# Performance work log

Measured on AMD Instinct MI355X. Metric: run time of the kernel, lower is better.

## Reference

```python
import jax, jax.numpy as jnp
import numpy as np

# ---- config (matches init_kwargs) ----
GROUP_NUM = 2048
K_NEIGHBORS = 32
OUT_DIM = 192
SIGMA, BASELINE, SCALING, EPS = 0.26, 0.1, 10.0, 1e-6
ALPHA, BETA = 1000.0, 100.0
ADAPTIVE_RATIO = 0.5
IN_DIM = 3
ADAPTIVE_DIM = int(OUT_DIM * ADAPTIVE_RATIO)          # 96
FOURIER_DIM = OUT_DIM - ADAPTIVE_DIM                  # 96
FEAT_DIM_F = FOURIER_DIM // (IN_DIM * 2)              # 16
FEAT_DIM_A = int(np.ceil(ADAPTIVE_DIM / IN_DIM))      # 32
FEAT_NUM_A = FEAT_DIM_A * IN_DIM                      # 96
OUT_IDX = np.linspace(0, FEAT_NUM_A - 1, ADAPTIVE_DIM).astype(np.int64)


def setup_inputs() -> dict:
    key = jax.random.key(0)
    k1, k2, k3, k4 = jax.random.split(key, 4)
    xyz = jax.random.normal(k1, (4, 8192, 3), dtype=jnp.float32)
    x = jax.random.normal(k2, (4, 8192, 96), dtype=jnp.float32)
    bn_gamma = jax.random.uniform(k3, (192,), dtype=jnp.float32)
    bn_beta = jax.random.normal(k4, (192,), dtype=jnp.float32)
    return {"xyz": xyz, "x": x, "bn_gamma": bn_gamma, "bn_beta": bn_beta}


def _fps(xyz, m):
    """Farthest point sampling. xyz: [B,N,3] -> idx [B,m] (int32). Seed = index 0."""
    def single(pts):
        n = pts.shape[0]
        def step(carry, _):
            dists, last = carry
            d = jnp.sum((pts - pts[last]) ** 2, axis=-1)
            dists = jnp.minimum(dists, d)
            nxt = jnp.argmax(dists).astype(jnp.int32)
            return (dists, nxt), nxt
        init = (jnp.full((n,), 1e10, pts.dtype), jnp.array(0, jnp.int32))
        _, idxs = jax.lax.scan(step, init, None, length=m - 1)
        return jnp.concatenate([jnp.zeros((1,), jnp.int32), idxs])
    return jax.vmap(single)(xyz)


def _square_distance(src, dst):
    # src: [B,S,3], dst: [B,N,3] -> [B,S,N]
    d = -2.0 * jnp.einsum('bsc,bnc->bsn', src, dst)
    d += jnp.sum(src ** 2, -1)[:, :, None]
    d += jnp.sum(dst ** 2, -1)[:, None, :]
    return d


def _gather_knn(points, idx):
    # points: [B,N,C], idx: [B,G,K] -> [B,G,K,C]
    return jax.vmap(lambda p, i: p[i])(points, idx)


def _forward(xyz, x, bn_gamma, bn_beta):
    B, N, _ = xyz.shape
    G, K = GROUP_NUM, K_NEIGHBORS

    # ---- Grouper_seg ----
    fps_idx = _fps(xyz, G)                                   # [B,G]
    lc_xyz = jnp.take_along_axis(xyz, fps_idx[..., None], 1)  # [B,G,3]
    lc_x = jnp.take_along_axis(x, fps_idx[..., None], 1)      # [B,G,C]
    sqr = _square_distance(lc_xyz, xyz)                       # [B,G,N]
    knn_idx = jax.lax.top_k(-sqr, K)[1]                       # [B,G,K] smallest-k
    knn_xyz = _gather_knn(xyz, knn_idx)                       # [B,G,K,3]
    knn_x = _gather_knn(x, knn_idx)                           # [B,G,K,C]

    # ---- Aggregation_seg: local normalization ----
    mean_x = lc_x[:, :, None, :]
    std_x = jnp.std(knn_x - mean_x, ddof=1)
    mean_xyz = lc_xyz[:, :, None, :]
    std_xyz = jnp.std(knn_xyz - mean_xyz, ddof=1)
    knn_x = (knn_x - mean_x) / (std_x + 1e-5)
    knn_xyz_n = (knn_xyz - mean_xyz) / (std_xyz + 1e-5)       # [B,G,K,3]
    C = knn_x.shape[-1]
    knn_x = jnp.concatenate(
        [knn_x, jnp.broadcast_to(lc_x[:, :, None, :], (B, G, K, C))], axis=-1)  # [B,G,K,2C]
    knn_xyz_cf = jnp.transpose(knn_xyz_n, (0, 3, 1, 2))       # [B,3,G,K]
    knn_x_cf = jnp.transpose(knn_x, (0, 3, 1, 2))             # [B,OUT_DIM,G,K]

    # ---- PosE_Geo: fourier part ----
    feat_range = jnp.arange(FEAT_DIM_F, dtype=knn_xyz_cf.dtype)
    dim_embed = ALPHA ** (feat_range / FEAT_DIM_F)            # [F]
    div = BETA * knn_xyz_cf[..., None] / dim_embed            # [B,3,G,K,F]
    fourier = jnp.stack([jnp.sin(div), jnp.cos(div)], axis=-1)  # [B,3,G,K,F,2]
    fourier = fourier.reshape(B, IN_DIM, G, K, 2 * FEAT_DIM_F)
    fourier = jnp.transpose(fourier, (0, 1, 4, 2, 3)).reshape(B, FOURIER_DIM, G, K)

    # ---- AdaptiveEmbedding (parameterless, data-driven) ----
    x4 = knn_xyz_n                                            # [B,G,K,3]
    gstd = jnp.mean(jnp.std(x4.reshape(B, -1, IN_DIM), axis=1, ddof=1))
    sig = SIGMA * (1.0 + gstd) + EPS
    blend = jax.nn.sigmoid((gstd - BASELINE) * SCALING)
    feat_val = jnp.linspace(-1.0, 1.0, FEAT_DIM_A + 2)[1:-1]  # [Fa]
    z = (x4[..., None] - feat_val) / sig                      # [B,G,K,3,Fa]
    comb = blend * jnp.exp(-0.5 * z * z) + (1.0 - blend) * jnp.cos(z)
    ae = comb.reshape(B, G, K, FEAT_NUM_A)[..., OUT_IDX]      # [B,G,K,ADAPTIVE_DIM]
    ae_cf = jnp.transpose(ae, (0, 3, 1, 2))                   # [B,ADAPTIVE_DIM,G,K]

    pe = jnp.concatenate([fourier, ae_cf], axis=1)            # [B,OUT_DIM,G,K]
    knn_x_w = (knn_x_cf + pe) * pe

    # ---- Pooling_seg: max+mean pool, BatchNorm1d (train stats) + GELU ----
    lc = jnp.max(knn_x_w, -1) + jnp.mean(knn_x_w, -1)         # [B,OUT_DIM,G]
    mu = jnp.mean(lc, axis=(0, 2), keepdims=True)
    var = jnp.var(lc, axis=(0, 2), keepdims=True)
    y = (lc - mu) / jnp.sqrt(var + 1e-5)
    y = y * bn_gamma[None, :, None] + bn_beta[None, :, None]
    return jax.nn.gelu(y, approximate=False)


def reference(xyz, x, bn_gamma, bn_beta):
    return _forward(xyz, x, bn_gamma, bn_beta)
```

## Files before the change

kernel.cpp:

```cpp
#include <hip/hip_runtime.h>
#include <cstdint>
#include <math.h>

#define NPTS 8192
#define NB 4
#define NG 2048
#define NK 32
#define CIN 96
#define COUT 192

typedef unsigned long long ull;

__global__ __launch_bounds__(256) void setup_kernel(const float* __restrict__ xyz,
                                                    float* __restrict__ xs, float* __restrict__ ys,
                                                    float* __restrict__ zs, float* __restrict__ d2){
  int i = blockIdx.x*256 + threadIdx.x;
  if (i >= NB*NPTS) return;
  float x = xyz[3*i+0], y = xyz[3*i+1], z = xyz[3*i+2];
  xs[i]=x; ys[i]=y; zs[i]=z;
  d2[i] = __fadd_rn(__fadd_rn(__fmul_rn(x,x),__fmul_rn(y,y)),__fmul_rn(z,z));
}

template<int CTRL>
__device__ __forceinline__ void dppmax_pair(unsigned& hi, unsigned& lo){
  unsigned ohi = (unsigned)__builtin_amdgcn_update_dpp((int)hi, (int)hi, CTRL, 0xf, 0xf, false);
  unsigned olo = (unsigned)__builtin_amdgcn_update_dpp((int)lo, (int)lo, CTRL, 0xf, 0xf, false);
  bool gt = (ohi > hi) || (ohi == hi && olo > lo);
  hi = gt ? ohi : hi;
  lo = gt ? olo : lo;
}

__device__ __forceinline__ ull umax64(ull a, ull b){ return (a > b) ? a : b; }
__device__ __forceinline__ unsigned umax32(unsigned a, unsigned b){ return (a > b) ? a : b; }

__global__ __launch_bounds__(512,2) void fps_kernel(const float* __restrict__ xyz, int* __restrict__ fps_idx){
#pragma clang fp contract(off)
  extern __shared__ char smem[];
  float4* ctab = (float4*)smem;
  ull*    keys = (ull*)(smem + 131072);
  int*    hist = (int*)(smem + 131072 + 128);
  float*  bbs  = (float*)(smem + 131072 + 128 + 2048);
  const int b = blockIdx.x, t = threadIdx.x;
  const int w = t>>6, lane = t&63;
  const float* base = xyz + (size_t)b*NPTS*3;

  float ox[16], oy[16], oz[16];
#pragma unroll
  for (int j=0;j<16;++j){
    int p = t + 512*j;
    ox[j]=base[3*p+0]; oy[j]=base[3*p+1]; oz[j]=base[3*p+2];
  }
  float mnx=ox[0],mxx=ox[0],mny=oy[0],mxy=oy[0],mnz=oz[0],mxz=oz[0];
#pragma unroll
  for (int j=1;j<16;++j){
    mnx=fminf(mnx,ox[j]); mxx=fmaxf(mxx,ox[j]);
    mny=fminf(mny,oy[j]); mxy=fmaxf(mxy,oy[j]);
    mnz=fminf(mnz,oz[j]); mxz=fmaxf(mxz,oz[j]);
  }
#pragma unroll
  for (int off=32; off>0; off>>=1){
    mnx=fminf(mnx,__shfl_xor(mnx,off)); mxx=fmaxf(mxx,__shfl_xor(mxx,off));
    mny=fminf(mny,__shfl_xor(mny,off)); mxy=fmaxf(mxy,__shfl_xor(mxy,off));
    mnz=fminf(mnz,__shfl_xor(mnz,off)); mxz=fmaxf(mxz,__shfl_xor(mxz,off));
  }
  hist[t] = 0;
  if (lane==0){
    bbs[w*6+0]=mnx; bbs[w*6+1]=mxx; bbs[w*6+2]=mny;
    bbs[w*6+3]=mxy; bbs[w*6+4]=mnz; bbs[w*6+5]=mxz;
  }
  if (t==0) fps_idx[b*NG] = 0;
  __syncthreads();
  float gx0=1e30f,gx1=-1e30f,gy0=1e30f,gy1=-1e30f,gz0=1e30f,gz1=-1e30f;
  for (int q=0;q<8;++q){
    gx0=fminf(gx0,bbs[q*6+0]); gx1=fmaxf(gx1,bbs[q*6+1]);
    gy0=fminf(gy0,bbs[q*6+2]); gy1=fmaxf(gy1,bbs[q*6+3]);
    gz0=fminf(gz0,bbs[q*6+4]); gz1=fmaxf(gz1,bbs[q*6+5]);
  }
  const float sxv = 8.0f/fmaxf(gx1-gx0,1e-20f);
  const float syv = 8.0f/fmaxf(gy1-gy0,1e-20f);
  const float szv = 8.0f/fmaxf(gz1-gz0,1e-20f);
  int cell[16];
#pragma unroll
  for (int j=0;j<16;++j){
    int cx = min(7,(int)((ox[j]-gx0)*sxv));
    int cy = min(7,(int)((oy[j]-gy0)*syv));
    int cz = min(7,(int)((oz[j]-gz0)*szv));
    int m = (cx&1) | ((cy&1)<<1) | ((cz&1)<<2)
          | ((cx&2)<<2) | ((cy&2)<<3) | ((cz&2)<<4)
          | ((cx&4)<<4) | ((cy&4)<<5) | ((cz&4)<<6);
    cell[j]=m;
    atomicAdd(&hist[m],1);
  }
  __syncthreads();
  if (t < 64){
    int s0[8];
#pragma unroll
    for (int j=0;j<8;++j) s0[j]=hist[t*8+j];
    int tot=0;
#pragma unroll
    for (int j=0;j<8;++j){ int v=s0[j]; s0[j]=tot; tot+=v; }
    int inc=tot;
#pragma unroll
    for (int off=1; off<64; off<<=1){
      int o=__shfl_up(inc,off);
      if (t>=off) inc+=o;
    }
    int excl=inc-tot;
#pragma unroll
    for (int j=0;j<8;++j) hist[t*8+j]=excl+s0[j];
  }
  __syncthreads();
#pragma unroll
  for (int j=0;j<16;++j){
    int pos = atomicAdd(&hist[cell[j]],1);
    ctab[pos] = make_float4(ox[j],oy[j],oz[j], __int_as_float(t+512*j));
  }
  __syncthreads();
  float px[16],py[16],pz[16],D[16]; unsigned lowb[16];
  float bx0,bx1,by0,by1,bz0,bz1;
#pragma unroll
  for (int j=0;j<16;++j){
    int pos = (w<<10) + (j<<6) + lane;
    float4 c4 = ctab[pos];
    px[j]=c4.x; py[j]=c4.y; pz[j]=c4.z;
    unsigned orig = (unsigned)__float_as_int(c4.w);
    lowb[j] = ((8191u-orig)<<13) | (unsigned)pos;
    D[j] = 1e10f;
    if (j==0){ bx0=c4.x; bx1=c4.x; by0=c4.y; by1=c4.y; bz0=c4.z; bz1=c4.z; }
    else {
      bx0=fminf(bx0,c4.x); bx1=fmaxf(bx1,c4.x);
      by0=fminf(by0,c4.y); by1=fmaxf(by1,c4.y);
      bz0=fminf(bz0,c4.z); bz1=fmaxf(bz1,c4.z);
    }
  }
#pragma unroll
  for (int off=32; off>0; off>>=1){
    bx0=fminf(bx0,__shfl_xor(bx0,off)); bx1=fmaxf(bx1,__shfl_xor(bx1,off));
    by0=fminf(by0,__shfl_xor(by0,off)); by1=fmaxf(by1,__shfl_xor(by1,off));
    bz0=fminf(bz0,__shfl_xor(bz0,off)); bz1=fmaxf(bz1,__shfl_xor(bz1,off));
  }

  float lx=base[0], ly=base[1], lz=base[2];
  float Mw = 1e10f;
  unsigned mylow = 0;
  for (int it=0; it<NG-1; ++it){
    float qx=fminf(fmaxf(lx,bx0),bx1);
    float qy=fminf(fmaxf(ly,by0),by1);
    float qz=fminf(fmaxf(lz,bz0),bz1);
    float ddx=qx-lx, ddy=qy-ly, ddz=qz-lz;
    float LB = (ddx*ddx+ddy*ddy)+ddz*ddz;
    ull* kslot = &keys[(it&1)*8 + w];
    if (LB <= Mw*1.0001f){
#pragma unroll
      for (int j=0;j<16;++j){
        float dx=px[j]-lx, dy=py[j]-ly, dz=pz[j]-lz;
        float d=(dx*dx+dy*dy)+dz*dz;
        D[j]=fminf(D[j],d);
      }
      float m0=fmaxf(D[0],D[1]),   m1=fmaxf(D[2],D[3]);
      float m2=fmaxf(D[4],D[5]),   m3=fmaxf(D[6],D[7]);
      float m4=fmaxf(D[8],D[9]),   m5=fmaxf(D[10],D[11]);
      float m6=fmaxf(D[12],D[13]), m7=fmaxf(D[14],D[15]);
      float n0=fmaxf(m0,m1), n1=fmaxf(m2,m3), n2=fmaxf(m4,m5), n3=fmaxf(m6,m7);
      float bd=fmaxf(fmaxf(n0,n1),fmaxf(n2,n3));
      unsigned c[16];
#pragma unroll
      for (int j=0;j<16;++j) c[j] = (D[j]==bd) ? lowb[j] : 0u;
      unsigned u0=umax32(c[0],c[1]),   u1=umax32(c[2],c[3]);
      unsigned u2=umax32(c[4],c[5]),   u3=umax32(c[6],c[7]);
      unsigned u4=umax32(c[8],c[9]),   u5=umax32(c[10],c[11]);
      unsigned u6=umax32(c[12],c[13]), u7=umax32(c[14],c[15]);
      unsigned v0=umax32(u0,u1), v1=umax32(u2,u3), v2=umax32(u4,u5), v3=umax32(u6,u7);
      unsigned bl=umax32(umax32(v0,v1),umax32(v2,v3));
      unsigned hi = __float_as_uint(bd), lo = bl;
      dppmax_pair<0x111>(hi,lo); dppmax_pair<0x112>(hi,lo); dppmax_pair<0x114>(hi,lo);
      dppmax_pair<0x118>(hi,lo); dppmax_pair<0x142>(hi,lo); dppmax_pair<0x143>(hi,lo);
      unsigned hw  = (unsigned)__builtin_amdgcn_readlane((int)hi,63);
      unsigned lwv = (unsigned)__builtin_amdgcn_readlane((int)lo,63);
      if (lane==63) *kslot = (((ull)hw)<<32) | (ull)lwv;
      Mw = __uint_as_float(hw);
      mylow = lwv;
    } else {
      if (lane==63) *kslot = (((ull)__float_as_uint(Mw))<<32) | (ull)mylow;
    }
    __syncthreads();
    const ulonglong2* kk2 = (const ulonglong2*)(keys + (it&1)*8);
    ulonglong2 p0 = kk2[0], p1 = kk2[1], p2 = kk2[2], p3 = kk2[3];
    ull a0 = umax64(p0.x, p0.y), a1 = umax64(p1.x, p1.y);
    ull a2 = umax64(p2.x, p2.y), a3 = umax64(p3.x, p3.y);
    ull k  = umax64(umax64(a0,a1), umax64(a2,a3));
    unsigned lw = (unsigned)k;
    float4 c4 = ctab[lw & 0x1FFFu];
    lx=c4.x; ly=c4.y; lz=c4.z;
    if (t==0) fps_idx[b*NG + it + 1] = (int)(8191u - ((lw>>13)&0x1FFFu));
  }
}

__device__ __forceinline__ bool lexlt(float ad, int ai, float bd, int bi){
  return (ad < bd) || ((ad == bd) && (ai < bi));
}
__device__ __forceinline__ void sort_desc(float& d, int& i, int lane){
#pragma unroll
  for (int k=2;k<=64;k<<=1){
#pragma unroll
    for (int j=k>>1;j>0;j>>=1){
      float od = __shfl_xor(d, j);
      int   oi = __shfl_xor(i, j);
      bool dirUp = (lane & k) != 0;
      bool lower = (lane & j) == 0;
      bool less  = lexlt(d,i,od,oi);
      bool keep  = (less == (lower == dirUp));
      if (!keep){ d=od; i=oi; }
    }
  }
}
__device__ __forceinline__ void merge_asc(float& d, int& i, int lane){
#pragma unroll
  for (int j=32;j>0;j>>=1){
    float od = __shfl_xor(d, j);
    int   oi = __shfl_xor(i, j);
    bool lower = (lane & j) == 0;
    bool less  = lexlt(d,i,od,oi);
    bool keep  = (less == lower);
    if (!keep){ d=od; i=oi; }
  }
}

__global__ __launch_bounds__(256) void knn_kernel(const float* __restrict__ xs, const float* __restrict__ ys,
                                                  const float* __restrict__ zs, const float* __restrict__ d2,
                                                  const int* __restrict__ fps_idx, int* __restrict__ knn_out){
  __shared__ float tx[256], ty[256], tz[256], td[256];
  const int tid = threadIdx.x;
  const int wid = tid>>6, lane = tid&63;
  const int pid = blockIdx.x*4 + wid;
  const int b = pid >> 11;
  const float* bx = xs + b*NPTS;
  const float* by = ys + b*NPTS;
  const float* bz = zs + b*NPTS;
  const float* bD = d2 + b*NPTS;
  const int fi = fps_idx[pid];
  const float ax = bx[fi], ay = by[fi], az = bz[fi];
  const float src2 = __fadd_rn(__fadd_rn(__fmul_rn(ax,ax),__fmul_rn(ay,ay)),__fmul_rn(az,az));
  float Ad = INFINITY; int Ai = 0x7fffffff;
  float tau_d = INFINITY; int tau_i = 0x7fffffff;
  for (int s=0; s<NPTS/256; ++s){
    __syncthreads();
    int gidx = s*256 + tid;
    tx[tid]=bx[gidx]; ty[tid]=by[gidx]; tz[tid]=bz[gidx]; td[tid]=bD[gidx];
    __syncthreads();
    float m0,m1,m2,m3; int i0,i1,i2,i3;
#define LOADJ(mj, ij, J) { int li = (J)*64 + lane; \
    float dot = __fadd_rn(__fadd_rn(__fmul_rn(ax,tx[li]),__fmul_rn(ay,ty[li])),__fmul_rn(az,tz[li])); \
    mj = __fadd_rn(__fadd_rn(__fmul_rn(-2.0f,dot), src2), td[li]); ij = s*256 + li; }
    LOADJ(m0,i0,0) LOADJ(m1,i1,1) LOADJ(m2,i2,2) LOADJ(m3,i3,3)
#undef LOADJ
    while (true){
      bool any = lexlt(m0,i0,tau_d,tau_i) || lexlt(m1,i1,tau_d,tau_i) ||
                 lexlt(m2,i2,tau_d,tau_i) || lexlt(m3,i3,tau_d,tau_i);
      if (__ballot(any) == 0ull) break;
      float cd = m0; int ci = i0; int sel = 0;
      if (lexlt(m1,i1,cd,ci)){ cd=m1; ci=i1; sel=1; }
      if (lexlt(m2,i2,cd,ci)){ cd=m2; ci=i2; sel=2; }
      if (lexlt(m3,i3,cd,ci)){ cd=m3; ci=i3; sel=3; }
      if      (sel==0) m0=INFINITY;
      else if (sel==1) m1=INFINITY;
      else if (sel==2) m2=INFINITY;
      else             m3=INFINITY;
      sort_desc(cd, ci, lane);
      if (lexlt(cd,ci,Ad,Ai)){ Ad=cd; Ai=ci; }
      merge_asc(Ad, Ai, lane);
      tau_d = __shfl(Ad, 31);
      tau_i = __shfl(Ai, 31);
    }
  }
  if (lane < NK) knn_out[pid*NK + lane] = Ai;
}

__global__ __launch_bounds__(256) void stats_kernel(const float* __restrict__ x, const float* __restrict__ xyz,
                                                    const int* __restrict__ fps_idx, const int* __restrict__ knn,
                                                    double* __restrict__ partials){
  const int tid=threadIdx.x, wid=tid>>6, lane=tid&63;
  const int pid = blockIdx.x*4 + wid;
  const int b = pid>>11;
  const int fi = fps_idx[pid];
  const float* xb = x + (size_t)b*NPTS*CIN;
  const float* zb = xyz + (size_t)b*NPTS*3;
  const float lc0 = xb[fi*CIN + lane];
  float lc1 = 0.f; if (lane<32) lc1 = xb[fi*CIN + 64 + lane];
  float czv = 0.f; if (lane<3)  czv = zb[fi*3 + lane];
  double s1=0.0, s2=0.0, a1=0.0, a2=0.0;
  for (int k=0;k<NK;++k){
    int idx = knn[pid*NK + k];
    float d0 = __fsub_rn(xb[idx*CIN + lane], lc0);
    s1 += (double)d0; s2 += (double)d0*(double)d0;
    if (lane<32){
      float d1 = __fsub_rn(xb[idx*CIN + 64 + lane], lc1);
      s1 += (double)d1; s2 += (double)d1*(double)d1;
    }
    if (lane<3){
      float w = __fsub_rn(zb[idx*3 + lane], czv);
      a1 += (double)w; a2 += (double)w*(double)w;
    }
  }
#pragma unroll
  for (int off=32; off>0; off>>=1){ s1 += __shfl_xor(s1,off); s2 += __shfl_xor(s2,off); }
  __shared__ double shx[4][2];
  __shared__ double shz[4][3][2];
  if (lane==0){ shx[wid][0]=s1; shx[wid][1]=s2; }
  if (lane<3){ shz[wid][lane][0]=a1; shz[wid][lane][1]=a2; }
  __syncthreads();
  if (tid==0){
    double u0=0,u1=0;
    for (int w=0;w<4;++w){ u0+=shx[w][0]; u1+=shx[w][1]; }
    double* outp = partials + (size_t)blockIdx.x*8;
    outp[0]=u0; outp[1]=u1;
    for (int axq=0; axq<3; ++axq){
      double v0=0,v1=0;
      for (int w=0;w<4;++w){ v0+=shz[w][axq][0]; v1+=shz[w][axq][1]; }
      outp[2+2*axq]=v0; outp[3+2*axq]=v1;
    }
  }
}

__global__ void finalize_kernel(const double* __restrict__ partials, float* __restrict__ scal){
  const int lane = threadIdx.x;
  double s1=0,s2=0;
  double z0a=0,z0b=0,z1a=0,z1b=0,z2a=0,z2b=0;
  for (int i=0;i<32;++i){
    const double* p = partials + (size_t)(lane*32+i)*8;
    s1+=p[0]; s2+=p[1];
    z0a+=p[2]; z0b+=p[3]; z1a+=p[4]; z1b+=p[5]; z2a+=p[6]; z2b+=p[7];
  }
#pragma unroll
  for (int off=32; off>0; off>>=1){ s1+=__shfl_xor(s1,off); s2+=__shfl_xor(s2,off); }
#pragma unroll
  for (int off=8; off>0; off>>=1){
    z0a+=__shfl_xor(z0a,off); z0b+=__shfl_xor(z0b,off);
    z1a+=__shfl_xor(z1a,off); z1b+=__shfl_xor(z1b,off);
    z2a+=__shfl_xor(z2a,off); z2b+=__shfl_xor(z2b,off);
  }
  __shared__ double zb[4][3][2];
  if ((lane&15)==0){
    int b = lane>>4;
    zb[b][0][0]=z0a; zb[b][0][1]=z0b;
    zb[b][1][0]=z1a; zb[b][1][1]=z1b;
    zb[b][2][0]=z2a; zb[b][2][1]=z2b;
  }
  __syncthreads();
  if (lane==0){
    double nx = (double)NB*NG*NK*CIN;
    double varx = (s2 - s1*s1/nx)/(nx-1.0);
    float stdx = (float)sqrt(varx);
    double t1=0,t2=0;
    for (int b=0;b<4;++b) for (int a=0;a<3;++a){ t1+=zb[b][a][0]; t2+=zb[b][a][1]; }
    double nz = (double)NB*NG*NK*3;
    double varz = (t2 - t1*t1/nz)/(nz-1.0);
    float stdz = (float)sqrt(varz);
    float sdiv = stdz + 1e-5f;
    double n2 = (double)NG*NK;
    double acc=0.0;
    for (int b=0;b<4;++b) for (int a=0;a<3;++a){
      double v = (zb[b][a][1] - zb[b][a][0]*zb[b][a][0]/n2)/(n2-1.0);
      acc += sqrt(v);
    }
    float gstd = (float)(acc/12.0) / sdiv;
    float sig = 0.26f*(1.0f+gstd) + 1e-6f;
    float blend = 1.0f/(1.0f + expf(-(gstd-0.1f)*10.0f));
    scal[0] = 1.0f/(stdx + 1e-5f);
    scal[1] = 1.0f/sdiv;
    scal[2] = 1.0f/sig;
    scal[3] = blend;
  }
}

__global__ __launch_bounds__(256) void main_kernel(const float* __restrict__ x, const float* __restrict__ xyz,
                                                   const int* __restrict__ fps_idx, const int* __restrict__ knn,
                                                   const float* __restrict__ scal, float* __restrict__ lc_out){
  const int tid=threadIdx.x, wid=tid>>6, lane=tid&63;
  const int pid = blockIdx.x*4 + wid;
  const int b = pid>>11, g = pid&2047;
  const float inv_x = scal[0], inv_z = scal[1], inv_sig = scal[2], blend = scal[3];
  const float omb = 1.0f - blend;
  const int fi = fps_idx[pid];
  const float* xb = x + (size_t)b*NPTS*CIN;
  const float* zb = xyz + (size_t)b*NPTS*3;
  const float cx = zb[fi*3+0], cy = zb[fi*3+1], cz = zb[fi*3+2];
  const float lcx0 = xb[fi*CIN + lane];
  const float lcx1 = (lane<32) ? xb[fi*CIN + 64 + lane] : xb[fi*CIN + lane - 32];
  const float lcx2 = xb[fi*CIN + 32 + lane];
  const int dim0 = lane>>5;
  const int rr0 = lane&31;
  const bool cos0 = rr0 & 1;
  const float bs0 = 100.0f / powf(1000.0f, (float)(rr0>>1) * (1.0f/16.0f));
  const bool cos1 = lane & 1;
  const float bs1 = 100.0f / powf(1000.0f, (float)((lane&31)>>1) * (1.0f/16.0f));
  const float fv1 = (float)(-1.0 + 2.0*(double)(lane-32+1)/33.0);
  const int dim2 = (32+lane)>>5;
  const int j2 = (32+lane)&31;
  const float fv2 = (float)(-1.0 + 2.0*(double)(j2+1)/33.0);

  float mx0=-INFINITY, mx1=-INFINITY, mx2=-INFINITY;
  float sm0=0.f, sm1=0.f, sm2=0.f;
  for (int k=0;k<NK;++k){
    const int idx = knn[pid*NK + k];
    const float p0 = zb[idx*3+0], p1 = zb[idx*3+1], p2v = zb[idx*3+2];
    const float xn0 = (p0-cx)*inv_z, xn1 = (p1-cy)*inv_z, xn2 = (p2v-cz)*inv_z;
    const float xk0 = xb[idx*CIN + lane];
    float xk1 = 0.f; if (lane<32) xk1 = xb[idx*CIN + 64 + lane];
    {
      float v = dim0 ? xn1 : xn0;
      float a = v * bs0;
      float pe = cos0 ? __cosf(a) : __sinf(a);
      float f = (xk0 - lcx0) * inv_x;
      float w = (f + pe) * pe;
      mx0 = fmaxf(mx0, w); sm0 += w;
    }
    {
      float pe, f;
      if (lane < 32){
        float a = xn2 * bs1;
        pe = cos1 ? __cosf(a) : __sinf(a);
        f = (xk1 - lcx1) * inv_x;
      } else {
        float zq = (xn0 - fv1) * inv_sig;
        pe = blend * __expf(-0.5f*zq*zq) + omb * __cosf(zq);
        f = lcx1;
      }
      float w = (f + pe) * pe;
      mx1 = fmaxf(mx1, w); sm1 += w;
    }
    {
      float v = (dim2==1) ? xn1 : xn2;
      float zq = (v - fv2) * inv_sig;
      float pe = blend * __expf(-0.5f*zq*zq) + omb * __cosf(zq);
      float w = (lcx2 + pe) * pe;
      mx2 = fmaxf(mx2, w); sm2 += w;
    }
  }
  const size_t obase = ((size_t)b*COUT)*NG + g;
  lc_out[obase + (size_t)lane*NG]       = mx0 + sm0*(1.0f/32.0f);
  lc_out[obase + (size_t)(64+lane)*NG]  = mx1 + sm1*(1.0f/32.0f);
  lc_out[obase + (size_t)(128+lane)*NG] = mx2 + sm2*(1.0f/32.0f);
}

__global__ __launch_bounds__(256) void bn_stats_kernel(const float* __restrict__ lc, float* __restrict__ bn){
  const int c = blockIdx.x, t = threadIdx.x, lane=t&63, wid=t>>6;
  double s1=0.0, s2=0.0;
  for (int i=t; i<NB*NG; i+=256){
    int b=i>>11, g=i&2047;
    float v = lc[((size_t)(b*COUT)+c)*NG + g];
    s1 += (double)v; s2 += (double)v*(double)v;
  }
#pragma unroll
  for (int off=32; off>0; off>>=1){ s1+=__shfl_xor(s1,off); s2+=__shfl_xor(s2,off); }
  __shared__ double sh1[4], sh2[4];
  if (lane==0){ sh1[wid]=s1; sh2[wid]=s2; }
  __syncthreads();
  if (t==0){
    double a=sh1[0]+sh1[1]+sh1[2]+sh1[3], q=sh2[0]+sh2[1]+sh2[2]+sh2[3];
    double n=(double)(NB*NG);
    double mu=a/n, var=q/n - mu*mu;
    bn[c]=(float)mu;
    bn[COUT+c]=(float)(1.0/sqrt(var + 1e-5));
  }
}

__global__ __launch_bounds__(256) void final_kernel(const float* __restrict__ bn, const float* __restrict__ gamma,
                                                    const float* __restrict__ beta, float* __restrict__ out){
  int i = blockIdx.x*256 + threadIdx.x;
  int c = (i >> 11) % COUT;
  float v = out[i];
  float y = (v - bn[c]) * bn[COUT + c];
  y = y*gamma[c] + beta[c];
  out[i] = y * 0.5f * (1.0f + erff(y * 0.70710678118654752f));
}

extern "C" void kernel_launch(void* const* d_in, const int* in_sizes, int n_in,
                              void* d_out, int out_size, void* d_ws, size_t ws_size,
                              hipStream_t stream){
  const float* xyz   = (const float*)d_in[0];
  const float* x     = (const float*)d_in[1];
  const float* gamma = (const float*)d_in[2];
  const float* beta  = (const float*)d_in[3];
  float* out = (float*)d_out;
  char* ws = (char*)d_ws;
  int*    fps  = (int*)   (ws + 0);
  int*    knn  = (int*)   (ws + 32768);
  float*  xs   = (float*) (ws + 1081344);
  float*  ys   = (float*) (ws + 1212416);
  float*  zs   = (float*) (ws + 1343488);
  float*  d2   = (float*) (ws + 1474560);
  double* parts= (double*)(ws + 1605632);
  float*  scal = (float*) (ws + 1736704);
  float*  bn   = (float*) (ws + 1736768);

  const int fps_lds = 131072 + 128 + 2048 + 192;
  (void)hipFuncSetAttribute(reinterpret_cast<const void*>(fps_kernel),
                            hipFuncAttributeMaxDynamicSharedMemorySize, fps_lds);

  setup_kernel   <<<dim3((NB*NPTS+255)/256), dim3(256), 0, stream>>>(xyz, xs, ys, zs, d2);
  fps_kernel     <<<dim3(NB),                dim3(512), fps_lds, stream>>>(xyz, fps);
  knn_kernel     <<<dim3(NB*NG/4),           dim3(256), 0, stream>>>(xs, ys, zs, d2, fps, knn);
  stats_kernel   <<<dim3(NB*NG/4),           dim3(256), 0, stream>>>(x, xyz, fps, knn, parts);
  finalize_kernel<<<dim3(1),                 dim3(64),  0, stream>>>(parts, scal);
  main_kernel    <<<dim3(NB*NG/4),           dim3(256), 0, stream>>>(x, xyz, fps, knn, scal, out);
  bn_stats_kernel<<<dim3(COUT),              dim3(256), 0, stream>>>(out, bn);
  final_kernel   <<<dim3((NB*COUT*NG)/256),  dim3(256), 0, stream>>>(bn, gamma, beta, out);
}
```

Before: 2.476 ms.

## Fuse FPS, KNN and stats into one ticketed kernel that overlaps FPS

Replaces the separate FPS, KNN and stats kernels with one kernel whose blocks take roles from an atomic ticket counter. The first four blocks run farthest point sampling and publish progress flags every 16 samples. The remaining blocks spin until their 8 centroids are ready, then run KNN and the per-group feature statistics, reading neighbour indices directly from registers. The aim is to hide KNN and stats behind the long serial FPS loop and drop two launches plus the knn index reload. The cost is that waiting blocks hold CUs with large LDS reservations, the design depends on ticket ordering for forward progress, and the partials ordering changes, so finalize is adjusted to match.

```diff
diff --git a/kernel.cpp b/kernel.cpp
--- a/kernel.cpp
+++ b/kernel.cpp
@@ -13,8 +13,10 @@
 
 __global__ __launch_bounds__(256) void setup_kernel(const float* __restrict__ xyz,
                                                     float* __restrict__ xs, float* __restrict__ ys,
-                                                    float* __restrict__ zs, float* __restrict__ d2){
+                                                    float* __restrict__ zs, float* __restrict__ d2,
+                                                    int* __restrict__ ctrs){
   int i = blockIdx.x*256 + threadIdx.x;
+  if (i < 8){ ctrs[i] = 0; }
   if (i >= NB*NPTS) return;
   float x = xyz[3*i+0], y = xyz[3*i+1], z = xyz[3*i+2];
   xs[i]=x; ys[i]=y; zs[i]=z;
@@ -32,169 +34,6 @@
 
 __device__ __forceinline__ ull umax64(ull a, ull b){ return (a > b) ? a : b; }
 __device__ __forceinline__ unsigned umax32(unsigned a, unsigned b){ return (a > b) ? a : b; }
-
-__global__ __launch_bounds__(512,2) void fps_kernel(const float* __restrict__ xyz, int* __restrict__ fps_idx){
-#pragma clang fp contract(off)
-  extern __shared__ char smem[];
-  float4* ctab = (float4*)smem;
-  ull*    keys = (ull*)(smem + 131072);
-  int*    hist = (int*)(smem + 131072 + 128);
-  float*  bbs  = (float*)(smem + 131072 + 128 + 2048);
-  const int b = blockIdx.x, t = threadIdx.x;
-  const int w = t>>6, lane = t&63;
-  const float* base = xyz + (size_t)b*NPTS*3;
-
-  float ox[16], oy[16], oz[16];
-#pragma unroll
-  for (int j=0;j<16;++j){
-    int p = t + 512*j;
-    ox[j]=base[3*p+0]; oy[j]=base[3*p+1]; oz[j]=base[3*p+2];
-  }
-  float mnx=ox[0],mxx=ox[0],mny=oy[0],mxy=oy[0],mnz=oz[0],mxz=oz[0];
-#pragma unroll
-  for (int j=1;j<16;++j){
-    mnx=fminf(mnx,ox[j]); mxx=fmaxf(mxx,ox[j]);
-    mny=fminf(mny,oy[j]); mxy=fmaxf(mxy,oy[j]);
-    mnz=fminf(mnz,oz[j]); mxz=fmaxf(mxz,oz[j]);
-  }
-#pragma unroll
-  for (int off=32; off>0; off>>=1){
-    mnx=fminf(mnx,__shfl_xor(mnx,off)); mxx=fmaxf(mxx,__shfl_xor(mxx,off));
-    mny=fminf(mny,__shfl_xor(mny,off)); mxy=fmaxf(mxy,__shfl_xor(mxy,off));
-    mnz=fminf(mnz,__shfl_xor(mnz,off)); mxz=fmaxf(mxz,__shfl_xor(mxz,off));
-  }
-  hist[t] = 0;
-  if (lane==0){
-    bbs[w*6+0]=mnx; bbs[w*6+1]=mxx; bbs[w*6+2]=mny;
-    bbs[w*6+3]=mxy; bbs[w*6+4]=mnz; bbs[w*6+5]=mxz;
-  }
-  if (t==0) fps_idx[b*NG] = 0;
-  __syncthreads();
-  float gx0=1e30f,gx1=-1e30f,gy0=1e30f,gy1=-1e30f,gz0=1e30f,gz1=-1e30f;
-  for (int q=0;q<8;++q){
-    gx0=fminf(gx0,bbs[q*6+0]); gx1=fmaxf(gx1,bbs[q*6+1]);
-    gy0=fminf(gy0,bbs[q*6+2]); gy1=fmaxf(gy1,bbs[q*6+3]);
-    gz0=fminf(gz0,bbs[q*6+4]); gz1=fmaxf(gz1,bbs[q*6+5]);
-  }
-  const float sxv = 8.0f/fmaxf(gx1-gx0,1e-20f);
-  const float syv = 8.0f/fmaxf(gy1-gy0,1e-20f);
-  const float szv = 8.0f/fmaxf(gz1-gz0,1e-20f);
-  int cell[16];
-#pragma unroll
-  for (int j=0;j<16;++j){
-    int cx = min(7,(int)((ox[j]-gx0)*sxv));
-    int cy = min(7,(int)((oy[j]-gy0)*syv));
-    int cz = min(7,(int)((oz[j]-gz0)*szv));
-    int m = (cx&1) | ((cy&1)<<1) | ((cz&1)<<2)
-          | ((cx&2)<<2) | ((cy&2)<<3) | ((cz&2)<<4)
-          | ((cx&4)<<4) | ((cy&4)<<5) | ((cz&4)<<6);
-    cell[j]=m;
-    atomicAdd(&hist[m],1);
-  }
-  __syncthreads();
-  if (t < 64){
-    int s0[8];
-#pragma unroll
-    for (int j=0;j<8;++j) s0[j]=hist[t*8+j];
-    int tot=0;
-#pragma unroll
-    for (int j=0;j<8;++j){ int v=s0[j]; s0[j]=tot; tot+=v; }
-    int inc=tot;
-#pragma unroll
-    for (int off=1; off<64; off<<=1){
-      int o=__shfl_up(inc,off);
-      if (t>=off) inc+=o;
-    }
-    int excl=inc-tot;
-#pragma unroll
-    for (int j=0;j<8;++j) hist[t*8+j]=excl+s0[j];
-  }
-  __syncthreads();
-#pragma unroll
-  for (int j=0;j<16;++j){
-    int pos = atomicAdd(&hist[cell[j]],1);
-    ctab[pos] = make_float4(ox[j],oy[j],oz[j], __int_as_float(t+512*j));
-  }
-  __syncthreads();
-  float px[16],py[16],pz[16],D[16]; unsigned lowb[16];
-  float bx0,bx1,by0,by1,bz0,bz1;
-#pragma unroll
-  for (int j=0;j<16;++j){
-    int pos = (w<<10) + (j<<6) + lane;
-    float4 c4 = ctab[pos];
-    px[j]=c4.x; py[j]=c4.y; pz[j]=c4.z;
-    unsigned orig = (unsigned)__float_as_int(c4.w);
-    lowb[j] = ((8191u-orig)<<13) | (unsigned)pos;
-    D[j] = 1e10f;
-    if (j==0){ bx0=c4.x; bx1=c4.x; by0=c4.y; by1=c4.y; bz0=c4.z; bz1=c4.z; }
-    else {
-      bx0=fminf(bx0,c4.x); bx1=fmaxf(bx1,c4.x);
-      by0=fminf(by0,c4.y); by1=fmaxf(by1,c4.y);
-      bz0=fminf(bz0,c4.z); bz1=fmaxf(bz1,c4.z);
-    }
-  }
-#pragma unroll
-  for (int off=32; off>0; off>>=1){
-    bx0=fminf(bx0,__shfl_xor(bx0,off)); bx1=fmaxf(bx1,__shfl_xor(bx1,off));
-    by0=fminf(by0,__shfl_xor(by0,off)); by1=fmaxf(by1,__shfl_xor(by1,off));
-    bz0=fminf(bz0,__shfl_xor(bz0,off)); bz1=fmaxf(bz1,__shfl_xor(bz1,off));
-  }
-
-  float lx=base[0], ly=base[1], lz=base[2];
-  float Mw = 1e10f;
-  unsigned mylow = 0;
-  for (int it=0; it<NG-1; ++it){
-    float qx=fminf(fmaxf(lx,bx0),bx1);
-    float qy=fminf(fmaxf(ly,by0),by1);
-    float qz=fminf(fmaxf(lz,bz0),bz1);
-    float ddx=qx-lx, ddy=qy-ly, ddz=qz-lz;
-    float LB = (ddx*ddx+ddy*ddy)+ddz*ddz;
-    ull* kslot = &keys[(it&1)*8 + w];
-    if (LB <= Mw*1.0001f){
-#pragma unroll
-      for (int j=0;j<16;++j){
-        float dx=px[j]-lx, dy=py[j]-ly, dz=pz[j]-lz;
-        float d=(dx*dx+dy*dy)+dz*dz;
-        D[j]=fminf(D[j],d);
-      }
-      float m0=fmaxf(D[0],D[1]),   m1=fmaxf(D[2],D[3]);
-      float m2=fmaxf(D[4],D[5]),   m3=fmaxf(D[6],D[7]);
-      float m4=fmaxf(D[8],D[9]),   m5=fmaxf(D[10],D[11]);
-      float m6=fmaxf(D[12],D[13]), m7=fmaxf(D[14],D[15]);
-      float n0=fmaxf(m0,m1), n1=fmaxf(m2,m3), n2=fmaxf(m4,m5), n3=fmaxf(m6,m7);
-      float bd=fmaxf(fmaxf(n0,n1),fmaxf(n2,n3));
-      unsigned c[16];
-#pragma unroll
-      for (int j=0;j<16;++j) c[j] = (D[j]==bd) ? lowb[j] : 0u;
-      unsigned u0=umax32(c[0],c[1]),   u1=umax32(c[2],c[3]);
-      unsigned u2=umax32(c[4],c[5]),   u3=umax32(c[6],c[7]);
-      unsigned u4=umax32(c[8],c[9]),   u5=umax32(c[10],c[11]);
-      unsigned u6=umax32(c[12],c[13]), u7=umax32(c[14],c[15]);
-      unsigned v0=umax32(u0,u1), v1=umax32(u2,u3), v2=umax32(u4,u5), v3=umax32(u6,u7);
-      unsigned bl=umax32(umax32(v0,v1),umax32(v2,v3));
-      unsigned hi = __float_as_uint(bd), lo = bl;
-      dppmax_pair<0x111>(hi,lo); dppmax_pair<0x112>(hi,lo); dppmax_pair<0x114>(hi,lo);
-      dppmax_pair<0x118>(hi,lo); dppmax_pair<0x142>(hi,lo); dppmax_pair<0x143>(hi,lo);
-      unsigned hw  = (unsigned)__builtin_amdgcn_readlane((int)hi,63);
-      unsigned lwv = (unsigned)__builtin_amdgcn_readlane((int)lo,63);
-      if (lane==63) *kslot = (((ull)hw)<<32) | (ull)lwv;
-      Mw = __uint_as_float(hw);
-      mylow = lwv;
-    } else {
-      if (lane==63) *kslot = (((ull)__float_as_uint(Mw))<<32) | (ull)mylow;
-    }
-    __syncthreads();
-    const ulonglong2* kk2 = (const ulonglong2*)(keys + (it&1)*8);
-    ulonglong2 p0 = kk2[0], p1 = kk2[1], p2 = kk2[2], p3 = kk2[3];
-    ull a0 = umax64(p0.x, p0.y), a1 = umax64(p1.x, p1.y);
-    ull a2 = umax64(p2.x, p2.y), a3 = umax64(p3.x, p3.y);
-    ull k  = umax64(umax64(a0,a1), umax64(a2,a3));
-    unsigned lw = (unsigned)k;
-    float4 c4 = ctab[lw & 0x1FFFu];
-    lx=c4.x; ly=c4.y; lz=c4.z;
-    if (t==0) fps_idx[b*NG + it + 1] = (int)(8191u - ((lw>>13)&0x1FFFu));
-  }
-}
 
 __device__ __forceinline__ bool lexlt(float ad, int ai, float bd, int bi){
   return (ad < bd) || ((ad == bd) && (ai < bi));
@@ -226,98 +65,292 @@
   }
 }
 
-__global__ __launch_bounds__(256) void knn_kernel(const float* __restrict__ xs, const float* __restrict__ ys,
-                                                  const float* __restrict__ zs, const float* __restrict__ d2,
-                                                  const int* __restrict__ fps_idx, int* __restrict__ knn_out){
-  __shared__ float tx[256], ty[256], tz[256], td[256];
-  const int tid = threadIdx.x;
-  const int wid = tid>>6, lane = tid&63;
-  const int pid = blockIdx.x*4 + wid;
-  const int b = pid >> 11;
-  const float* bx = xs + b*NPTS;
-  const float* by = ys + b*NPTS;
-  const float* bz = zs + b*NPTS;
-  const float* bD = d2 + b*NPTS;
-  const int fi = fps_idx[pid];
-  const float ax = bx[fi], ay = by[fi], az = bz[fi];
-  const float src2 = __fadd_rn(__fadd_rn(__fmul_rn(ax,ax),__fmul_rn(ay,ay)),__fmul_rn(az,az));
-  float Ad = INFINITY; int Ai = 0x7fffffff;
-  float tau_d = INFINITY; int tau_i = 0x7fffffff;
-  for (int s=0; s<NPTS/256; ++s){
+__global__ __launch_bounds__(512,2) void mega_kernel(const float* __restrict__ xyz,
+                                                     const float* __restrict__ x,
+                                                     const float* __restrict__ xs,
+                                                     const float* __restrict__ ys,
+                                                     const float* __restrict__ zs,
+                                                     const float* __restrict__ d2,
+                                                     int* __restrict__ fps_idx,
+                                                     int* __restrict__ knn_out,
+                                                     double* __restrict__ partials,
+                                                     int* __restrict__ ctrs){
+  extern __shared__ char smem[];
+  __shared__ int role_s;
+  const int t = threadIdx.x;
+  const int w = t>>6, lane = t&63;
+  if (t==0) role_s = atomicAdd(&ctrs[0], 1);
+  __syncthreads();
+  const int ticket = role_s;
+
+  if (ticket < NB){
+#pragma clang fp contract(off)
+    float4* ctab = (float4*)smem;
+    ull*    keys = (ull*)(smem + 131072);
+    int*    hist = (int*)(smem + 131072 + 128);
+    float*  bbs  = (float*)(smem + 131072 + 128 + 2048);
+    const int b = ticket;
+    const float* base = xyz + (size_t)b*NPTS*3;
+
+    float ox[16], oy[16], oz[16];
+#pragma unroll
+    for (int j=0;j<16;++j){
+      int p = t + 512*j;
+      ox[j]=base[3*p+0]; oy[j]=base[3*p+1]; oz[j]=base[3*p+2];
+    }
+    float mnx=ox[0],mxx=ox[0],mny=oy[0],mxy=oy[0],mnz=oz[0],mxz=oz[0];
+#pragma unroll
+    for (int j=1;j<16;++j){
+      mnx=fminf(mnx,ox[j]); mxx=fmaxf(mxx,ox[j]);
+      mny=fminf(mny,oy[j]); mxy=fmaxf(mxy,oy[j]);
+      mnz=fminf(mnz,oz[j]); mxz=fmaxf(mxz,oz[j]);
+    }
+#pragma unroll
+    for (int off=32; off>0; off>>=1){
+      mnx=fminf(mnx,__shfl_xor(mnx,off)); mxx=fmaxf(mxx,__shfl_xor(mxx,off));
+      mny=fminf(mny,__shfl_xor(mny,off)); mxy=fmaxf(mxy,__shfl_xor(mxy,off));
+      mnz=fminf(mnz,__shfl_xor(mnz,off)); mxz=fmaxf(mxz,__shfl_xor(mxz,off));
+    }
+    hist[t] = 0;
+    if (lane==0){
+      bbs[w*6+0]=mnx; bbs[w*6+1]=mxx; bbs[w*6+2]=mny;
+      bbs[w*6+3]=mxy; bbs[w*6+4]=mnz; bbs[w*6+5]=mxz;
+    }
+    if (t==0) fps_idx[b*NG] = 0;
     __syncthreads();
-    int gidx = s*256 + tid;
-    tx[tid]=bx[gidx]; ty[tid]=by[gidx]; tz[tid]=bz[gidx]; td[tid]=bD[gidx];
+    float gx0=1e30f,gx1=-1e30f,gy0=1e30f,gy1=-1e30f,gz0=1e30f,gz1=-1e30f;
+    for (int q=0;q<8;++q){
+      gx0=fminf(gx0,bbs[q*6+0]); gx1=fmaxf(gx1,bbs[q*6+1]);
+      gy0=fminf(gy0,bbs[q*6+2]); gy1=fmaxf(gy1,bbs[q*6+3]);
+      gz0=fminf(gz0,bbs[q*6+4]); gz1=fmaxf(gz1,bbs[q*6+5]);
+    }
+    const float sxv = 8.0f/fmaxf(gx1-gx0,1e-20f);
+    const float syv = 8.0f/fmaxf(gy1-gy0,1e-20f);
+    const float szv = 8.0f/fmaxf(gz1-gz0,1e-20f);
+    int cell[16];
+#pragma unroll
+    for (int j=0;j<16;++j){
+      int cx = min(7,(int)((ox[j]-gx0)*sxv));
+      int cy = min(7,(int)((oy[j]-gy0)*syv));
+      int cz = min(7,(int)((oz[j]-gz0)*szv));
+      int m = (cx&1) | ((cy&1)<<1) | ((cz&1)<<2)
+            | ((cx&2)<<2) | ((cy&2)<<3) | ((cz&2)<<4)
+            | ((cx&4)<<4) | ((cy&4)<<5) | ((cz&4)<<6);
+      cell[j]=m;
+      atomicAdd(&hist[m],1);
+    }
     __syncthreads();
-    float m0,m1,m2,m3; int i0,i1,i2,i3;
+    if (t < 64){
+      int s0[8];
+#pragma unroll
+      for (int j=0;j<8;++j) s0[j]=hist[t*8+j];
+      int tot=0;
+#pragma unroll
+      for (int j=0;j<8;++j){ int v=s0[j]; s0[j]=tot; tot+=v; }
+      int inc=tot;
+#pragma unroll
+      for (int off=1; off<64; off<<=1){
+        int o=__shfl_up(inc,off);
+        if (t>=off) inc+=o;
+      }
+      int excl=inc-tot;
+#pragma unroll
+      for (int j=0;j<8;++j) hist[t*8+j]=excl+s0[j];
+    }
+    __syncthreads();
+#pragma unroll
+    for (int j=0;j<16;++j){
+      int pos = atomicAdd(&hist[cell[j]],1);
+      ctab[pos] = make_float4(ox[j],oy[j],oz[j], __int_as_float(t+512*j));
+    }
+    __syncthreads();
+    float px[16],py[16],pz[16],D[16]; unsigned lowb[16];
+    float bx0,bx1,by0,by1,bz0,bz1;
+#pragma unroll
+    for (int j=0;j<16;++j){
+      int pos = (w<<10) + (j<<6) + lane;
+      float4 c4 = ctab[pos];
+      px[j]=c4.x; py[j]=c4.y; pz[j]=c4.z;
+      unsigned orig = (unsigned)__float_as_int(c4.w);
+      lowb[j] = ((8191u-orig)<<13) | (unsigned)pos;
+      D[j] = 1e10f;
+      if (j==0){ bx0=c4.x; bx1=c4.x; by0=c4.y; by1=c4.y; bz0=c4.z; bz1=c4.z; }
+      else {
+        bx0=fminf(bx0,c4.x); bx1=fmaxf(bx1,c4.x);
+        by0=fminf(by0,c4.y); by1=fmaxf(by1,c4.y);
+        bz0=fminf(bz0,c4.z); bz1=fmaxf(bz1,c4.z);
+      }
+    }
+#pragma unroll
+    for (int off=32; off>0; off>>=1){
+      bx0=fminf(bx0,__shfl_xor(bx0,off)); bx1=fmaxf(bx1,__shfl_xor(bx1,off));
+      by0=fminf(by0,__shfl_xor(by0,off)); by1=fmaxf(by1,__shfl_xor(by1,off));
+      bz0=fminf(bz0,__shfl_xor(bz0,off)); bz1=fmaxf(bz1,__shfl_xor(bz1,off));
+    }
+
+    float lx=base[0], ly=base[1], lz=base[2];
+    float Mw = 1e10f;
+    unsigned mylow = 0;
+    for (int it=0; it<NG-1; ++it){
+      float qx=fminf(fmaxf(lx,bx0),bx1);
+      float qy=fminf(fmaxf(ly,by0),by1);
+      float qz=fminf(fmaxf(lz,bz0),bz1);
+      float ddx=qx-lx, ddy=qy-ly, ddz=qz-lz;
+      float LB = (ddx*ddx+ddy*ddy)+ddz*ddz;
+      ull* kslot = &keys[(it&1)*8 + w];
+      if (LB <= Mw*1.0001f){
+#pragma unroll
+        for (int j=0;j<16;++j){
+          float dx=px[j]-lx, dy=py[j]-ly, dz=pz[j]-lz;
+          float d=(dx*dx+dy*dy)+dz*dz;
+          D[j]=fminf(D[j],d);
+        }
+        float m0=fmaxf(D[0],D[1]),   m1=fmaxf(D[2],D[3]);
+        float m2=fmaxf(D[4],D[5]),   m3=fmaxf(D[6],D[7]);
+        float m4=fmaxf(D[8],D[9]),   m5=fmaxf(D[10],D[11]);
+        float m6=fmaxf(D[12],D[13]), m7=fmaxf(D[14],D[15]);
+        float n0=fmaxf(m0,m1), n1=fmaxf(m2,m3), n2=fmaxf(m4,m5), n3=fmaxf(m6,m7);
+        float bd=fmaxf(fmaxf(n0,n1),fmaxf(n2,n3));
+        unsigned c[16];
+#pragma unroll
+        for (int j=0;j<16;++j) c[j] = (D[j]==bd) ? lowb[j] : 0u;
+        unsigned u0=umax32(c[0],c[1]),   u1=umax32(c[2],c[3]);
+        unsigned u2=umax32(c[4],c[5]),   u3=umax32(c[6],c[7]);
+        unsigned u4=umax32(c[8],c[9]),   u5=umax32(c[10],c[11]);
+        unsigned u6=umax32(c[12],c[13]), u7=umax32(c[14],c[15]);
+        unsigned v0=umax32(u0,u1), v1=umax32(u2,u3), v2=umax32(u4,u5), v3=umax32(u6,u7);
+        unsigned bl=umax32(umax32(v0,v1),umax32(v2,v3));
+        unsigned hi = __float_as_uint(bd), lo = bl;
+        dppmax_pair<0x111>(hi,lo); dppmax_pair<0x112>(hi,lo); dppmax_pair<0x114>(hi,lo);
+        dppmax_pair<0x118>(hi,lo); dppmax_pair<0x142>(hi,lo); dppmax_pair<0x143>(hi,lo);
+        unsigned hw  = (unsigned)__builtin_amdgcn_readlane((int)hi,63);
+        unsigned lwv = (unsigned)__builtin_amdgcn_readlane((int)lo,63);
+        if (lane==63) *kslot = (((ull)hw)<<32) | (ull)lwv;
+        Mw = __uint_as_float(hw);
+        mylow = lwv;
+      } else {
+        if (lane==63) *kslot = (((ull)__float_as_uint(Mw))<<32) | (ull)mylow;
+      }
+      __syncthreads();
+      const ulonglong2* kk2 = (const ulonglong2*)(keys + (it&1)*8);
+      ulonglong2 p0 = kk2[0], p1 = kk2[1], p2 = kk2[2], p3 = kk2[3];
+      ull a0 = umax64(p0.x, p0.y), a1 = umax64(p1.x, p1.y);
+      ull a2 = umax64(p2.x, p2.y), a3 = umax64(p3.x, p3.y);
+      ull k  = umax64(umax64(a0,a1), umax64(a2,a3));
+      unsigned lw = (unsigned)k;
+      float4 c4 = ctab[lw & 0x1FFFu];
+      lx=c4.x; ly=c4.y; lz=c4.z;
+      if (t==0){
+        fps_idx[b*NG + it + 1] = (int)(8191u - ((lw>>13)&0x1FFFu));
+        if (((it+2)&15)==0)
+          __hip_atomic_store(&ctrs[1+b], it+2, __ATOMIC_RELEASE, __HIP_MEMORY_SCOPE_AGENT);
+      }
+    }
+  } else {
+    const int cc = ticket - NB;
+    const int b  = cc & 3;
+    const int chunk = cc >> 2;
+    const int g0 = chunk*8;
+    if (t==0){
+      while (__hip_atomic_load(&ctrs[1+b], __ATOMIC_ACQUIRE, __HIP_MEMORY_SCOPE_AGENT) < g0+8)
+        __builtin_amdgcn_s_sleep(8);
+    }
+    __syncthreads();
+    const int g   = g0 + w;
+    const int pid = b*NG + g;
+    const int fi  = fps_idx[pid];
+
+    float* tx = (float*)smem;
+    float* ty = tx + 512;
+    float* tz = ty + 512;
+    float* td = tz + 512;
+    const float* bx = xs + b*NPTS;
+    const float* by = ys + b*NPTS;
+    const float* bz = zs + b*NPTS;
+    const float* bD = d2 + b*NPTS;
+    const float ax = bx[fi], ay = by[fi], az = bz[fi];
+    const float src2 = __fadd_rn(__fadd_rn(__fmul_rn(ax,ax),__fmul_rn(ay,ay)),__fmul_rn(az,az));
+    float Ad = INFINITY; int Ai = 0x7fffffff;
+    float tau_d = INFINITY; int tau_i = 0x7fffffff;
+    for (int s=0; s<NPTS/512; ++s){
+      __syncthreads();
+      int gidx = s*512 + t;
+      tx[t]=bx[gidx]; ty[t]=by[gidx]; tz[t]=bz[gidx]; td[t]=bD[gidx];
+      __syncthreads();
+      float m0,m1,m2,m3,m4,m5,m6,m7; int i0,i1,i2,i3,i4,i5,i6,i7;
 #define LOADJ(mj, ij, J) { int li = (J)*64 + lane; \
-    float dot = __fadd_rn(__fadd_rn(__fmul_rn(ax,tx[li]),__fmul_rn(ay,ty[li])),__fmul_rn(az,tz[li])); \
-    mj = __fadd_rn(__fadd_rn(__fmul_rn(-2.0f,dot), src2), td[li]); ij = s*256 + li; }
-    LOADJ(m0,i0,0) LOADJ(m1,i1,1) LOADJ(m2,i2,2) LOADJ(m3,i3,3)
+      float dot = __fadd_rn(__fadd_rn(__fmul_rn(ax,tx[li]),__fmul_rn(ay,ty[li])),__fmul_rn(az,tz[li])); \
+      mj = __fadd_rn(__fadd_rn(__fmul_rn(-2.0f,dot), src2), td[li]); ij = s*512 + li; }
+      LOADJ(m0,i0,0) LOADJ(m1,i1,1) LOADJ(m2,i2,2) LOADJ(m3,i3,3)
+      LOADJ(m4,i4,4) LOADJ(m5,i5,5) LOADJ(m6,i6,6) LOADJ(m7,i7,7)
 #undef LOADJ
-    while (true){
-      bool any = lexlt(m0,i0,tau_d,tau_i) || lexlt(m1,i1,tau_d,tau_i) ||
-                 lexlt(m2,i2,tau_d,tau_i) || lexlt(m3,i3,tau_d,tau_i);
-      if (__ballot(any) == 0ull) break;
-      float cd = m0; int ci = i0; int sel = 0;
-      if (lexlt(m1,i1,cd,ci)){ cd=m1; ci=i1; sel=1; }
-      if (lexlt(m2,i2,cd,ci)){ cd=m2; ci=i2; sel=2; }
-      if (lexlt(m3,i3,cd,ci)){ cd=m3; ci=i3; sel=3; }
-      if      (sel==0) m0=INFINITY;
-      else if (sel==1) m1=INFINITY;
-      else if (sel==2) m2=INFINITY;
-      else             m3=INFINITY;
-      sort_desc(cd, ci, lane);
-      if (lexlt(cd,ci,Ad,Ai)){ Ad=cd; Ai=ci; }
-      merge_asc(Ad, Ai, lane);
-      tau_d = __shfl(Ad, 31);
-      tau_i = __shfl(Ai, 31);
-    }
-  }
-  if (lane < NK) knn_out[pid*NK + lane] = Ai;
-}
-
-__global__ __launch_bounds__(256) void stats_kernel(const float* __restrict__ x, const float* __restrict__ xyz,
-                                                    const int* __restrict__ fps_idx, const int* __restrict__ knn,
-                                                    double* __restrict__ partials){
-  const int tid=threadIdx.x, wid=tid>>6, lane=tid&63;
-  const int pid = blockIdx.x*4 + wid;
-  const int b = pid>>11;
-  const int fi = fps_idx[pid];
-  const float* xb = x + (size_t)b*NPTS*CIN;
-  const float* zb = xyz + (size_t)b*NPTS*3;
-  const float lc0 = xb[fi*CIN + lane];
-  float lc1 = 0.f; if (lane<32) lc1 = xb[fi*CIN + 64 + lane];
-  float czv = 0.f; if (lane<3)  czv = zb[fi*3 + lane];
-  double s1=0.0, s2=0.0, a1=0.0, a2=0.0;
-  for (int k=0;k<NK;++k){
-    int idx = knn[pid*NK + k];
-    float d0 = __fsub_rn(xb[idx*CIN + lane], lc0);
-    s1 += (double)d0; s2 += (double)d0*(double)d0;
-    if (lane<32){
-      float d1 = __fsub_rn(xb[idx*CIN + 64 + lane], lc1);
-      s1 += (double)d1; s2 += (double)d1*(double)d1;
-    }
-    if (lane<3){
-      float w = __fsub_rn(zb[idx*3 + lane], czv);
-      a1 += (double)w; a2 += (double)w*(double)w;
-    }
-  }
-#pragma unroll
-  for (int off=32; off>0; off>>=1){ s1 += __shfl_xor(s1,off); s2 += __shfl_xor(s2,off); }
-  __shared__ double shx[4][2];
-  __shared__ double shz[4][3][2];
-  if (lane==0){ shx[wid][0]=s1; shx[wid][1]=s2; }
-  if (lane<3){ shz[wid][lane][0]=a1; shz[wid][lane][1]=a2; }
-  __syncthreads();
-  if (tid==0){
-    double u0=0,u1=0;
-    for (int w=0;w<4;++w){ u0+=shx[w][0]; u1+=shx[w][1]; }
-    double* outp = partials + (size_t)blockIdx.x*8;
-    outp[0]=u0; outp[1]=u1;
-    for (int axq=0; axq<3; ++axq){
-      double v0=0,v1=0;
-      for (int w=0;w<4;++w){ v0+=shz[w][axq][0]; v1+=shz[w][axq][1]; }
-      outp[2+2*axq]=v0; outp[3+2*axq]=v1;
+      while (true){
+        bool any = lexlt(m0,i0,tau_d,tau_i) || lexlt(m1,i1,tau_d,tau_i) ||
+                   lexlt(m2,i2,tau_d,tau_i) || lexlt(m3,i3,tau_d,tau_i) ||
+                   lexlt(m4,i4,tau_d,tau_i) || lexlt(m5,i5,tau_d,tau_i) ||
+                   lexlt(m6,i6,tau_d,tau_i) || lexlt(m7,i7,tau_d,tau_i);
+        if (__ballot(any) == 0ull) break;
+        float cd = m0; int ci = i0; int sel = 0;
+        if (lexlt(m1,i1,cd,ci)){ cd=m1; ci=i1; sel=1; }
+        if (lexlt(m2,i2,cd,ci)){ cd=m2; ci=i2; sel=2; }
+        if (lexlt(m3,i3,cd,ci)){ cd=m3; ci=i3; sel=3; }
+        if (lexlt(m4,i4,cd,ci)){ cd=m4; ci=i4; sel=4; }
+        if (lexlt(m5,i5,cd,ci)){ cd=m5; ci=i5; sel=5; }
+        if (lexlt(m6,i6,cd,ci)){ cd=m6; ci=i6; sel=6; }
+        if (lexlt(m7,i7,cd,ci)){ cd=m7; ci=i7; sel=7; }
+        if      (sel==0) m0=INFINITY;
+        else if (sel==1) m1=INFINITY;
+        else if (sel==2) m2=INFINITY;
+        else if (sel==3) m3=INFINITY;
+        else if (sel==4) m4=INFINITY;
+        else if (sel==5) m5=INFINITY;
+        else if (sel==6) m6=INFINITY;
+        else             m7=INFINITY;
+        sort_desc(cd, ci, lane);
+        if (lexlt(cd,ci,Ad,Ai)){ Ad=cd; Ai=ci; }
+        merge_asc(Ad, Ai, lane);
+        tau_d = __shfl(Ad, 31);
+        tau_i = __shfl(Ai, 31);
+      }
+    }
+    if (lane < NK) knn_out[pid*NK + lane] = Ai;
+
+    const float* xb  = x   + (size_t)b*NPTS*CIN;
+    const float* zbp = xyz + (size_t)b*NPTS*3;
+    const float lc0 = xb[fi*CIN + lane];
+    float lc1 = 0.f; if (lane<32) lc1 = xb[fi*CIN + 64 + lane];
+    float czv = 0.f; if (lane<3)  czv = zbp[fi*3 + lane];
+    double s1=0.0, s2=0.0, a1=0.0, a2=0.0;
+    for (int kk=0;kk<NK;++kk){
+      int idx = __shfl(Ai, kk);
+      float d0 = __fsub_rn(xb[idx*CIN + lane], lc0);
+      s1 += (double)d0; s2 += (double)d0*(double)d0;
+      if (lane<32){
+        float d1 = __fsub_rn(xb[idx*CIN + 64 + lane], lc1);
+        s1 += (double)d1; s2 += (double)d1*(double)d1;
+      }
+      if (lane<3){
+        float wv = __fsub_rn(zbp[idx*3 + lane], czv);
+        a1 += (double)wv; a2 += (double)wv*(double)wv;
+      }
+    }
+#pragma unroll
+    for (int off=32; off>0; off>>=1){ s1 += __shfl_xor(s1,off); s2 += __shfl_xor(s2,off); }
+    __shared__ double shx[8][2];
+    __shared__ double shz[8][3][2];
+    if (lane==0){ shx[w][0]=s1; shx[w][1]=s2; }
+    if (lane<3){ shz[w][lane][0]=a1; shz[w][lane][1]=a2; }
+    __syncthreads();
+    if (t==0){
+      double u0=0,u1=0;
+      for (int q=0;q<8;++q){ u0+=shx[q][0]; u1+=shx[q][1]; }
+      double* outp = partials + (size_t)cc*8;
+      outp[0]=u0; outp[1]=u1;
+      for (int axq=0; axq<3; ++axq){
+        double v0=0,v1=0;
+        for (int q=0;q<8;++q){ v0+=shz[q][axq][0]; v1+=shz[q][axq][1]; }
+        outp[2+2*axq]=v0; outp[3+2*axq]=v1;
+      }
     }
   }
 }
@@ -326,8 +359,9 @@
   const int lane = threadIdx.x;
   double s1=0,s2=0;
   double z0a=0,z0b=0,z1a=0,z1b=0,z2a=0,z2b=0;
-  for (int i=0;i<32;++i){
-    const double* p = partials + (size_t)(lane*32+i)*8;
+  const int bb = lane>>4, jj = lane&15;
+  for (int i=0;i<16;++i){
+    const double* p = partials + (size_t)(bb + 4*(jj*16 + i))*8;
     s1+=p[0]; s2+=p[1];
     z0a+=p[2]; z0b+=p[3]; z1a+=p[4]; z1b+=p[5]; z2a+=p[6]; z2b+=p[7];
   }
@@ -491,17 +525,17 @@
   float*  zs   = (float*) (ws + 1343488);
   float*  d2   = (float*) (ws + 1474560);
   double* parts= (double*)(ws + 1605632);
+  int*    ctrs = (int*)   (ws + 1671168);
   float*  scal = (float*) (ws + 1736704);
   float*  bn   = (float*) (ws + 1736768);
 
-  const int fps_lds = 131072 + 128 + 2048 + 192;
-  (void)hipFuncSetAttribute(reinterpret_cast<const void*>(fps_kernel),
-                            hipFuncAttributeMaxDynamicSharedMemorySize, fps_lds);
-
-  setup_kernel   <<<dim3((NB*NPTS+255)/256), dim3(256), 0, stream>>>(xyz, xs, ys, zs, d2);
-  fps_kernel     <<<dim3(NB),                dim3(512), fps_lds, stream>>>(xyz, fps);
-  knn_kernel     <<<dim3(NB*NG/4),           dim3(256), 0, stream>>>(xs, ys, zs, d2, fps, knn);
-  stats_kernel   <<<dim3(NB*NG/4),           dim3(256), 0, stream>>>(x, xyz, fps, knn, parts);
+  const int mega_lds = 131072 + 128 + 2048 + 192;
+  (void)hipFuncSetAttribute(reinterpret_cast<const void*>(mega_kernel),
+                            hipFuncAttributeMaxDynamicSharedMemorySize, mega_lds);
+
+  setup_kernel   <<<dim3((NB*NPTS+255)/256), dim3(256), 0, stream>>>(xyz, xs, ys, zs, d2, ctrs);
+  mega_kernel    <<<dim3(NB + NB*NG/8),      dim3(512), mega_lds, stream>>>(xyz, x, xs, ys, zs, d2,
+                                                                            fps, knn, parts, ctrs);
   finalize_kernel<<<dim3(1),                 dim3(64),  0, stream>>>(parts, scal);
   main_kernel    <<<dim3(NB*NG/4),           dim3(256), 0, stream>>>(x, xyz, fps, knn, scal, out);
   bn_stats_kernel<<<dim3(COUT),              dim3(256), 0, stream>>>(out, bn);
```

Result: slower. 4.025 ms (+62.6%).
